# Kernel optimization log

Measured on AMD Instinct MI355X. Metric: run time of the kernel, lower is better.

## Reference

```python
import jax, jax.numpy as jnp
import numpy as np

T, H, NH, NKV, HD = 2048, 1024, 16, 4, 64
I, E, TOPK = 2048, 8, 2
EPS = 1e-5
ROPE_BASE = 10000.0


def rms_norm(x, w):
    var = jnp.mean(x * x, axis=-1, keepdims=True)
    return x * jax.lax.rsqrt(var + EPS) * w


def apply_rope(x, positions, n_heads):
    # neox-style rotary over full head_dim
    t = x.reshape(-1, n_heads, HD)
    half = HD // 2
    inv_freq = 1.0 / (ROPE_BASE ** (jnp.arange(0, half, dtype=jnp.float32) / half))
    freqs = positions.astype(jnp.float32)[:, None] * inv_freq[None, :]  # [T, half]
    cos = jnp.cos(freqs)[:, None, :]
    sin = jnp.sin(freqs)[:, None, :]
    x1, x2 = t[..., :half], t[..., half:]
    rot = jnp.concatenate([x1 * cos - x2 * sin, x2 * cos + x1 * sin], axis=-1)
    return rot.reshape(x.shape)


def setup_inputs():
    key = jax.random.key(0)
    ks = jax.random.split(key, 9)
    s = 0.02
    return dict(
        positions=jnp.arange(T, dtype=jnp.int32),
        hidden_states=jax.random.normal(ks[0], (T, H), jnp.float32),
        input_ln_w=jnp.ones((H,), jnp.float32),
        post_ln_w=jnp.ones((H,), jnp.float32),
        residual_ln_w=jnp.ones((H,), jnp.float32),
        qkv_w=jax.random.normal(ks[1], ((NH + 2 * NKV) * HD, H), jnp.float32) * s,
        o_w=jax.random.normal(ks[2], (H, NH * HD), jnp.float32) * s,
        gate_w=jax.random.normal(ks[3], (E, H), jnp.float32) * s,
        ws=jax.random.normal(ks[4], (E, 2 * I, H), jnp.float32) * s,
        w2s=jax.random.normal(ks[5], (E, H, I), jnp.float32) * s,
        res_w13=jax.random.normal(ks[6], (2 * H, H), jnp.float32) * s,
        res_w2=jax.random.normal(ks[7], (H, H), jnp.float32) * s,
    )


def attention(x, positions, qkv_w, o_w):
    qkv = x @ qkv_w.T  # [T, (NH+2*NKV)*HD]
    q, k, v = jnp.split(qkv, [NH * HD, NH * HD + NKV * HD], axis=-1)
    q = apply_rope(q, positions, NH)
    k = apply_rope(k, positions, NKV)
    q = q.reshape(T, NH, HD)
    k = k.reshape(T, NKV, HD)
    v = v.reshape(T, NKV, HD)
    rep = NH // NKV  # GQA: repeat kv heads
    k = jnp.repeat(k, rep, axis=1)
    v = jnp.repeat(v, rep, axis=1)
    scale = HD ** -0.5
    scores = jnp.einsum('tnd,snd->nts', q, k) * scale  # [NH, T, T]
    causal = jnp.tril(jnp.ones((T, T), dtype=bool))
    scores = jnp.where(causal[None], scores, -jnp.inf)
    probs = jax.nn.softmax(scores, axis=-1)
    out = jnp.einsum('nts,snd->tnd', probs, v).reshape(T, NH * HD)
    return out @ o_w.T


def silu_and_mul(gu):
    g, u = jnp.split(gu, 2, axis=-1)
    return jax.nn.silu(g) * u


def moe(x, gate_w, ws, w2s):
    logits = x @ gate_w.T  # [T, E]
    probs = jax.nn.softmax(logits, axis=-1)
    topk_w, topk_ids = jax.lax.top_k(probs, TOPK)
    topk_w = topk_w / jnp.sum(topk_w, axis=-1, keepdims=True)  # renormalize (top_k > 1)
    routes = jnp.zeros((x.shape[0], E), x.dtype).at[
        jnp.arange(x.shape[0])[:, None], topk_ids].set(topk_w)  # [T, E] sparse routing
    gu = jnp.einsum('th,eih->tei', x, ws)        # [T, E, 2I]
    act = silu_and_mul(gu)                        # [T, E, I]
    eo = jnp.einsum('tei,ehi->teh', act, w2s)     # [T, E, H]
    return jnp.einsum('te,teh->th', routes, eo)


def reference(positions, hidden_states, input_ln_w, post_ln_w, residual_ln_w,
              qkv_w, o_w, gate_w, ws, w2s, res_w13, res_w2):
    residual_input = hidden_states
    h = rms_norm(hidden_states, input_ln_w)
    h = attention(h, positions, qkv_w, o_w)
    residual_attn = residual_input + h
    # parallel residual MLP branch (ffn_dim == hidden)
    r = rms_norm(residual_attn, residual_ln_w)
    r = silu_and_mul(r @ res_w13.T) @ res_w2.T
    residual_mlp = residual_attn + r
    # MoE branch
    m = rms_norm(residual_attn, post_ln_w)
    m = moe(m, gate_w, ws, w2s)
    return residual_mlp + m
```

## Files before the change

### kernel.cpp

```cpp
#include <hip/hip_runtime.h>
#include <stdint.h>


typedef _Float16 f16;
typedef _Float16 f16x8 __attribute__((ext_vector_type(8)));
typedef _Float16 f16x4 __attribute__((ext_vector_type(4)));
typedef float f32x4 __attribute__((ext_vector_type(4)));

#define DEV __device__ __forceinline__

DEV void glds16(const void* g, void* l) {
  __builtin_amdgcn_global_load_lds((const __attribute__((address_space(1))) void*)g,
                                   (__attribute__((address_space(3))) void*)l, 16, 0, 0);
}

__global__ void cvt_f16_kernel(const float* __restrict__ in, f16* __restrict__ outp) {
  const size_t i = ((size_t)blockIdx.x * 256 + threadIdx.x) * 4;
  float4 f = *(const float4*)(in + i);
  f16x4 o;
  o[0] = (f16)f.x; o[1] = (f16)f.y; o[2] = (f16)f.z; o[3] = (f16)f.w;
  *(f16x4*)(outp + i) = o;
}

__global__ void cvt_f16x2_kernel(const float* __restrict__ in,
                                 f16* __restrict__ oh, f16* __restrict__ ol) {
  const size_t i = ((size_t)blockIdx.x * 256 + threadIdx.x) * 4;
  float4 f = *(const float4*)(in + i);
  f16x4 h, l;
  h[0] = (f16)f.x; l[0] = (f16)(f.x - (float)h[0]);
  h[1] = (f16)f.y; l[1] = (f16)(f.y - (float)h[1]);
  h[2] = (f16)f.z; l[2] = (f16)(f.z - (float)h[2]);
  h[3] = (f16)f.w; l[3] = (f16)(f.w - (float)h[3]);
  *(f16x4*)(oh + i) = h;
  *(f16x4*)(ol + i) = l;
}

__global__ void rmsnorm_kernel(const float* __restrict__ in, const float* __restrict__ w,
                               f16* __restrict__ outp) {
  const int t = blockIdx.x * 4 + (threadIdx.x >> 6);
  const int lane = threadIdx.x & 63;
  const float* x = in + (size_t)t * 1024;
  float v[16]; float ss = 0.f;
#pragma unroll
  for (int j = 0; j < 16; j++) { float a = x[lane + 64 * j]; v[j] = a; ss += a * a; }
#pragma unroll
  for (int m = 1; m < 64; m <<= 1) ss += __shfl_xor(ss, m);
  const float rs = rsqrtf(ss * (1.f / 1024.f) + 1e-5f);
#pragma unroll
  for (int j = 0; j < 16; j++)
    outp[(size_t)t * 1024 + lane + 64 * j] = (f16)(v[j] * rs * w[lane + 64 * j]);
}

__global__ void rmsnorm_dual_kernel(const float* __restrict__ in,
                                    const float* __restrict__ w1, const float* __restrict__ w2,
                                    f16* __restrict__ o1, f16* __restrict__ o2) {
  const int t = blockIdx.x * 4 + (threadIdx.x >> 6);
  const int lane = threadIdx.x & 63;
  const float* x = in + (size_t)t * 1024;
  float v[16]; float ss = 0.f;
#pragma unroll
  for (int j = 0; j < 16; j++) { float a = x[lane + 64 * j]; v[j] = a; ss += a * a; }
#pragma unroll
  for (int m = 1; m < 64; m <<= 1) ss += __shfl_xor(ss, m);
  const float rs = rsqrtf(ss * (1.f / 1024.f) + 1e-5f);
#pragma unroll
  for (int j = 0; j < 16; j++) {
    float nv = v[j] * rs;
    size_t idx = (size_t)t * 1024 + lane + 64 * j;
    o1[idx] = (f16)(nv * w1[lane + 64 * j]);
    o2[idx] = (f16)(nv * w2[lane + 64 * j]);
  }
}

template <int EPI, int BN, int SPLITK = 1>
__global__ __launch_bounds__(256) void gemm_f16_kernel(
    const f16* __restrict__ A, const f16* __restrict__ B,
    void* __restrict__ outp, const float* __restrict__ addsrc,
    int M, int N, int K) {
  constexpr int JT = BN / 32;
  constexpr int L = (BN == 128) ? 4 : 3;
  __shared__ __attribute__((aligned(16))) f16 As[3][128 * 32];
  __shared__ __attribute__((aligned(16))) f16 Bs[3][BN * 32];
  const int tid = threadIdx.x;
  const size_t row0 = (size_t)blockIdx.y * 128, col0 = (size_t)blockIdx.x * BN;
  const int ks = (SPLITK > 1) ? (int)blockIdx.z : 0;
  const int kspan = K / SPLITK, kb = ks * kspan;
  const int nt = kspan >> 5;
  const int c0 = tid, c1 = tid + 256;
  const int sw0 = ((c0 & 3) ^ ((c0 >> 3) & 3)) * 8;
  const int sw1 = ((c1 & 3) ^ ((c1 >> 3) & 3)) * 8;
  const f16* a0 = A + (row0 + (c0 >> 2)) * K + sw0;
  const f16* a1 = A + (row0 + (c1 >> 2)) * K + sw1;
  const f16* b0 = B + (col0 + (c0 >> 2)) * K + sw0;
  const f16* b1 = B + (col0 + ((BN == 128) ? (c1 >> 2) : 0)) * K + ((BN == 128) ? sw1 : 0);

  const int wave = tid >> 6, lane = tid & 63, lr = lane >> 4, lc = lane & 15;
  const int wr = wave >> 1, wc = wave & 1;
  const int rsw = (lr ^ ((lc >> 1) & 3)) * 8;

  f32x4 acc[4][JT];
#pragma unroll
  for (int i = 0; i < 4; i++)
#pragma unroll
    for (int j = 0; j < JT; j++) acc[i][j] = (f32x4){0.f, 0.f, 0.f, 0.f};

  auto stage = [&](int k0, int buf) {
    glds16(a0 + k0, As[buf] + c0 * 8);
    glds16(a1 + k0, As[buf] + c1 * 8);
    glds16(b0 + k0, Bs[buf] + c0 * 8);
    if constexpr (BN == 128) glds16(b1 + k0, Bs[buf] + c1 * 8);
  };

  stage(kb, 0); stage(kb + 32, 1);
  for (int t = 0; t < nt; ++t) {
    if (t < nt - 1) asm volatile("s_waitcnt vmcnt(%0)" :: "n"(L) : "memory");
    else            asm volatile("s_waitcnt vmcnt(0)" ::: "memory");
    __builtin_amdgcn_s_barrier();
    asm volatile("" ::: "memory");
    if (t + 2 < nt) stage(kb + (t + 2) * 32, (t + 2) % 3);
    const f16* Ab = As[t % 3];
    const f16* Bb = Bs[t % 3];
    f16x8 af[4], bfr[JT];
#pragma unroll
    for (int i = 0; i < 4; i++)
      af[i] = *(const f16x8*)(Ab + (wr * 64 + i * 16 + lc) * 32 + rsw);
#pragma unroll
    for (int j = 0; j < JT; j++)
      bfr[j] = *(const f16x8*)(Bb + (wc * (BN / 2) + j * 16 + lc) * 32 + rsw);
#pragma unroll
    for (int i = 0; i < 4; i++)
#pragma unroll
      for (int j = 0; j < JT; j++)
        acc[i][j] = __builtin_amdgcn_mfma_f32_16x16x32_f16(af[i], bfr[j], acc[i][j], 0, 0, 0);
  }

#pragma unroll
  for (int i = 0; i < 4; i++)
#pragma unroll
    for (int j = 0; j < JT; j++) {
      const size_t rbase = row0 + wr * 64 + i * 16 + lr * 4;
      const size_t col = col0 + wc * (BN / 2) + j * 16 + lc;
#pragma unroll
      for (int r = 0; r < 4; r++) {
        size_t idx = (rbase + r) * N + col;
        if constexpr (SPLITK > 1) {
          ((float*)outp)[(size_t)ks * M * N + idx] = acc[i][j][r];
        } else if constexpr (EPI == 0) ((float*)outp)[idx] = acc[i][j][r];
        else if constexpr (EPI == 1) ((float*)outp)[idx] = acc[i][j][r] + addsrc[idx];
        else ((f16*)outp)[idx] = (f16)acc[i][j][r];
      }
    }
}

template <int SPLITK>
__global__ __launch_bounds__(256) void gemm_f16x2_add_kernel(
    const f16* __restrict__ Ah, const f16* __restrict__ Al,
    const f16* __restrict__ Bh, const f16* __restrict__ Bl,
    float* __restrict__ outp, const float* __restrict__ addsrc,
    int M, int N, int K) {
  __shared__ __attribute__((aligned(16))) f16 Ash[3][128 * 32];
  __shared__ __attribute__((aligned(16))) f16 Asl[3][128 * 32];
  __shared__ __attribute__((aligned(16))) f16 Bsh[3][64 * 32];
  __shared__ __attribute__((aligned(16))) f16 Bsl[3][64 * 32];
  const int tid = threadIdx.x;
  const size_t row0 = (size_t)blockIdx.y * 128, col0 = (size_t)blockIdx.x * 64;
  const int ks = (SPLITK > 1) ? (int)blockIdx.z : 0;
  const int kspan = K / SPLITK, kb = ks * kspan;
  const int nt = kspan >> 5;
  const int c0 = tid, c1 = tid + 256;
  const int sw0 = ((c0 & 3) ^ ((c0 >> 3) & 3)) * 8;
  const int sw1 = ((c1 & 3) ^ ((c1 >> 3) & 3)) * 8;
  const size_t aoff0 = (row0 + (c0 >> 2)) * K + sw0;
  const size_t aoff1 = (row0 + (c1 >> 2)) * K + sw1;
  const size_t boff0 = (col0 + (c0 >> 2)) * K + sw0;

  const int wave = tid >> 6, lane = tid & 63, lr = lane >> 4, lc = lane & 15;
  const int wr = wave >> 1, wc = wave & 1;
  const int rsw = (lr ^ ((lc >> 1) & 3)) * 8;

  f32x4 acc[4][2];
#pragma unroll
  for (int i = 0; i < 4; i++)
#pragma unroll
    for (int j = 0; j < 2; j++) acc[i][j] = (f32x4){0.f, 0.f, 0.f, 0.f};

  auto stage = [&](int k0, int buf) {
    glds16(Ah + aoff0 + k0, Ash[buf] + c0 * 8);
    glds16(Ah + aoff1 + k0, Ash[buf] + c1 * 8);
    glds16(Al + aoff0 + k0, Asl[buf] + c0 * 8);
    glds16(Al + aoff1 + k0, Asl[buf] + c1 * 8);
    glds16(Bh + boff0 + k0, Bsh[buf] + c0 * 8);
    glds16(Bl + boff0 + k0, Bsl[buf] + c0 * 8);
  };

  stage(kb, 0); stage(kb + 32, 1);
  for (int t = 0; t < nt; ++t) {
    if (t < nt - 1) asm volatile("s_waitcnt vmcnt(%0)" :: "n"(6) : "memory");
    else            asm volatile("s_waitcnt vmcnt(0)" ::: "memory");
    __builtin_amdgcn_s_barrier();
    asm volatile("" ::: "memory");
    if (t + 2 < nt) stage(kb + (t + 2) * 32, (t + 2) % 3);
    const int bc = t % 3;
    f16x8 afh[4], afl[4], bfh[2], bfl[2];
#pragma unroll
    for (int i = 0; i < 4; i++) {
      const int ro = (wr * 64 + i * 16 + lc) * 32 + rsw;
      afh[i] = *(const f16x8*)(Ash[bc] + ro);
      afl[i] = *(const f16x8*)(Asl[bc] + ro);
    }
#pragma unroll
    for (int j = 0; j < 2; j++) {
      const int ro = (wc * 32 + j * 16 + lc) * 32 + rsw;
      bfh[j] = *(const f16x8*)(Bsh[bc] + ro);
      bfl[j] = *(const f16x8*)(Bsl[bc] + ro);
    }
#pragma unroll
    for (int i = 0; i < 4; i++)
#pragma unroll
      for (int j = 0; j < 2; j++) {
        acc[i][j] = __builtin_amdgcn_mfma_f32_16x16x32_f16(afh[i], bfh[j], acc[i][j], 0, 0, 0);
        acc[i][j] = __builtin_amdgcn_mfma_f32_16x16x32_f16(afh[i], bfl[j], acc[i][j], 0, 0, 0);
        acc[i][j] = __builtin_amdgcn_mfma_f32_16x16x32_f16(afl[i], bfh[j], acc[i][j], 0, 0, 0);
      }
  }

#pragma unroll
  for (int i = 0; i < 4; i++)
#pragma unroll
    for (int j = 0; j < 2; j++) {
      const size_t rbase = row0 + wr * 64 + i * 16 + lr * 4;
      const size_t col = col0 + wc * 32 + j * 16 + lc;
#pragma unroll
      for (int r = 0; r < 4; r++) {
        size_t idx = (rbase + r) * N + col;
        if constexpr (SPLITK > 1) outp[(size_t)ks * M * N + idx] = acc[i][j][r];
        else outp[idx] = acc[i][j][r] + addsrc[idx];
      }
    }
}

__global__ __launch_bounds__(256) void gemm_moe_gated_kernel(
    const f16* __restrict__ A, const f16* __restrict__ Ball, f16* __restrict__ actm,
    const int* __restrict__ perm, const int* __restrict__ counts,
    int K, size_t strideB) {
  const int e = (int)blockIdx.z;
  const int cnt = counts[e];
  const int bm = blockIdx.y;
  if (bm * 128 >= cnt) return;
  const int nt = K >> 5;
  const f16* B = Ball + (size_t)e * strideB;
  __shared__ __attribute__((aligned(16))) f16 As[3][128 * 32];
  __shared__ __attribute__((aligned(16))) f16 Bgs[3][64 * 32];
  __shared__ __attribute__((aligned(16))) f16 Bus[3][64 * 32];
  const int tid = threadIdx.x;
  const size_t col0 = (size_t)blockIdx.x * 64;
  const int c0 = tid, c1 = tid + 256;
  const int pbase = e * 2048 + bm * 128;
  const int rt0 = c0 >> 2, rt1 = c1 >> 2;
  const int sid0 = (bm * 128 + rt0 < cnt) ? perm[pbase + rt0] : 0;
  const int sid1 = (bm * 128 + rt1 < cnt) ? perm[pbase + rt1] : 0;
  const size_t ar0 = (size_t)(sid0 >> 1);
  const size_t ar1 = (size_t)(sid1 >> 1);
  const int sw0 = ((c0 & 3) ^ ((c0 >> 3) & 3)) * 8;
  const int sw1 = ((c1 & 3) ^ ((c1 >> 3) & 3)) * 8;
  const f16* ap0 = A + ar0 * K + sw0;
  const f16* ap1 = A + ar1 * K + sw1;
  const f16* bg0 = B + (col0 + (c0 >> 2)) * K + sw0;
  const f16* bu0 = B + (2048 + col0 + (c0 >> 2)) * K + sw0;

  const int wave = tid >> 6, lane = tid & 63, lr = lane >> 4, lc = lane & 15;
  const int wr = wave >> 1, wc = wave & 1;
  const int rsw = (lr ^ ((lc >> 1) & 3)) * 8;

  f32x4 accg[4][2], accu[4][2];
#pragma unroll
  for (int i = 0; i < 4; i++)
#pragma unroll
    for (int j = 0; j < 2; j++) {
      accg[i][j] = (f32x4){0.f, 0.f, 0.f, 0.f};
      accu[i][j] = (f32x4){0.f, 0.f, 0.f, 0.f};
    }

  auto stage = [&](int k0, int buf) {
    glds16(ap0 + k0, As[buf] + c0 * 8);
    glds16(ap1 + k0, As[buf] + c1 * 8);
    glds16(bg0 + k0, Bgs[buf] + c0 * 8);
    glds16(bu0 + k0, Bus[buf] + c0 * 8);
  };

  stage(0, 0); stage(32, 1);
  for (int t = 0; t < nt; ++t) {
    if (t < nt - 1) asm volatile("s_waitcnt vmcnt(%0)" :: "n"(4) : "memory");
    else            asm volatile("s_waitcnt vmcnt(0)" ::: "memory");
    __builtin_amdgcn_s_barrier();
    asm volatile("" ::: "memory");
    if (t + 2 < nt) stage((t + 2) * 32, (t + 2) % 3);
    const f16* Ab = As[t % 3];
    const f16* Bgb = Bgs[t % 3];
    const f16* Bub = Bus[t % 3];
    f16x8 af[4], bg[2], bu[2];
#pragma unroll
    for (int i = 0; i < 4; i++)
      af[i] = *(const f16x8*)(Ab + (wr * 64 + i * 16 + lc) * 32 + rsw);
#pragma unroll
    for (int j = 0; j < 2; j++) {
      const int ro = (wc * 32 + j * 16 + lc) * 32 + rsw;
      bg[j] = *(const f16x8*)(Bgb + ro);
      bu[j] = *(const f16x8*)(Bub + ro);
    }
    __builtin_amdgcn_s_setprio(1);
#pragma unroll
    for (int i = 0; i < 4; i++)
#pragma unroll
      for (int j = 0; j < 2; j++) {
        accg[i][j] = __builtin_amdgcn_mfma_f32_16x16x32_f16(af[i], bg[j], accg[i][j], 0, 0, 0);
        accu[i][j] = __builtin_amdgcn_mfma_f32_16x16x32_f16(af[i], bu[j], accu[i][j], 0, 0, 0);
      }
    __builtin_amdgcn_s_setprio(0);
  }

  int sids[4][4];
#pragma unroll
  for (int i = 0; i < 4; i++)
#pragma unroll
    for (int r = 0; r < 4; r++) {
      int rit = wr * 64 + i * 16 + lr * 4 + r;
      sids[i][r] = (bm * 128 + rit < cnt) ? perm[pbase + rit] : -1;
    }
#pragma unroll
  for (int i = 0; i < 4; i++)
#pragma unroll
    for (int j = 0; j < 2; j++) {
      const size_t col = col0 + wc * 32 + j * 16 + lc;
#pragma unroll
      for (int r = 0; r < 4; r++)
        if (sids[i][r] >= 0) {
          const float g = accg[i][j][r], u = accu[i][j][r];
          actm[(size_t)sids[i][r] * 2048 + col] = (f16)(g / (1.f + __expf(-g)) * u);
        }
    }
}

template <int DIVROW, int BN, int SPLITK = 1>
__global__ __launch_bounds__(256) void gemm_moe_kernel(
    const f16* __restrict__ A, const f16* __restrict__ Ball, void* __restrict__ outp,
    const int* __restrict__ perm, const int* __restrict__ counts,
    int N, int K, size_t strideB) {
  constexpr int JT = BN / 32;
  constexpr int L = (BN == 128) ? 4 : 3;
  const int e = (int)blockIdx.z / SPLITK;
  const int ks = (int)blockIdx.z % SPLITK;
  const int cnt = counts[e];
  const int bm = blockIdx.y;
  if (bm * 128 >= cnt) return;
  const int kspan = K / SPLITK, kb = ks * kspan;
  const int nt = kspan >> 5;
  const f16* B = Ball + (size_t)e * strideB;
  __shared__ __attribute__((aligned(16))) f16 As[3][128 * 32];
  __shared__ __attribute__((aligned(16))) f16 Bs[3][BN * 32];
  const int tid = threadIdx.x;
  const size_t col0 = (size_t)blockIdx.x * BN;
  const int c0 = tid, c1 = tid + 256;
  const int pbase = e * 2048 + bm * 128;
  const int rt0 = c0 >> 2, rt1 = c1 >> 2;
  const int sid0 = (bm * 128 + rt0 < cnt) ? perm[pbase + rt0] : 0;
  const int sid1 = (bm * 128 + rt1 < cnt) ? perm[pbase + rt1] : 0;
  const size_t ar0 = DIVROW ? (size_t)(sid0 >> 1) : (size_t)sid0;
  const size_t ar1 = DIVROW ? (size_t)(sid1 >> 1) : (size_t)sid1;
  const int sw0 = ((c0 & 3) ^ ((c0 >> 3) & 3)) * 8;
  const int sw1 = ((c1 & 3) ^ ((c1 >> 3) & 3)) * 8;
  const f16* ap0 = A + ar0 * K + sw0;
  const f16* ap1 = A + ar1 * K + sw1;
  const f16* b0 = B + (col0 + (c0 >> 2)) * K + sw0;
  const f16* b1 = B + (col0 + ((BN == 128) ? (c1 >> 2) : 0)) * K + ((BN == 128) ? sw1 : 0);

  const int wave = tid >> 6, lane = tid & 63, lr = lane >> 4, lc = lane & 15;
  const int wr = wave >> 1, wc = wave & 1;
  const int rsw = (lr ^ ((lc >> 1) & 3)) * 8;

  f32x4 acc[4][JT];
#pragma unroll
  for (int i = 0; i < 4; i++)
#pragma unroll
    for (int j = 0; j < JT; j++) acc[i][j] = (f32x4){0.f, 0.f, 0.f, 0.f};

  auto stage = [&](int k0, int buf) {
    glds16(ap0 + k0, As[buf] + c0 * 8);
    glds16(ap1 + k0, As[buf] + c1 * 8);
    glds16(b0 + k0, Bs[buf] + c0 * 8);
    if constexpr (BN == 128) glds16(b1 + k0, Bs[buf] + c1 * 8);
  };

  stage(kb, 0); stage(kb + 32, 1);
  for (int t = 0; t < nt; ++t) {
    if (t < nt - 1) asm volatile("s_waitcnt vmcnt(%0)" :: "n"(L) : "memory");
    else            asm volatile("s_waitcnt vmcnt(0)" ::: "memory");
    __builtin_amdgcn_s_barrier();
    asm volatile("" ::: "memory");
    if (t + 2 < nt) stage(kb + (t + 2) * 32, (t + 2) % 3);
    const f16* Ab = As[t % 3];
    const f16* Bb = Bs[t % 3];
    f16x8 af[4], bfr[JT];
#pragma unroll
    for (int i = 0; i < 4; i++)
      af[i] = *(const f16x8*)(Ab + (wr * 64 + i * 16 + lc) * 32 + rsw);
#pragma unroll
    for (int j = 0; j < JT; j++)
      bfr[j] = *(const f16x8*)(Bb + (wc * (BN / 2) + j * 16 + lc) * 32 + rsw);
    __builtin_amdgcn_s_setprio(1);
#pragma unroll
    for (int i = 0; i < 4; i++)
#pragma unroll
      for (int j = 0; j < JT; j++)
        acc[i][j] = __builtin_amdgcn_mfma_f32_16x16x32_f16(af[i], bfr[j], acc[i][j], 0, 0, 0);
    __builtin_amdgcn_s_setprio(0);
  }

  int sids[4][4];
#pragma unroll
  for (int i = 0; i < 4; i++)
#pragma unroll
    for (int r = 0; r < 4; r++) {
      int rit = wr * 64 + i * 16 + lr * 4 + r;
      sids[i][r] = (bm * 128 + rit < cnt) ? perm[pbase + rit] : -1;
    }
#pragma unroll
  for (int i = 0; i < 4; i++)
#pragma unroll
    for (int j = 0; j < JT; j++) {
      const size_t col = col0 + wc * (BN / 2) + j * 16 + lc;
#pragma unroll
      for (int r = 0; r < 4; r++)
        if (sids[i][r] >= 0) {
          if constexpr (SPLITK > 1)
            ((float*)outp)[((size_t)ks * 4096 + sids[i][r]) * N + col] = acc[i][j][r];
          else
            ((f16*)outp)[(size_t)sids[i][r] * N + col] = (f16)acc[i][j][r];
        }
    }
}

__global__ void rope_table_kernel(const int* __restrict__ pos, float2* __restrict__ tab) {
  const int idx = blockIdx.x * 256 + threadIdx.x;
  const int t = idx >> 5, i = idx & 31;
  const double ph = (double)pos[t] * exp((double)i * -0.28782313662425575);
  tab[idx] = make_float2((float)cos(ph), (float)sin(ph));
}

__global__ void rope_kernel(const float* __restrict__ qkv, const float2* __restrict__ tab,
                            f16* __restrict__ qr, f16* __restrict__ kr) {
  const int t = blockIdx.y;
  const int u = blockIdx.x * 256 + threadIdx.x;
  if (u >= 640) return;
  const float* b0 = qkv + (size_t)t * 1536;
  const float* b1 = b0 + (size_t)2048 * 1536;
  const int head = u >> 5, i = u & 31;
  const bool isq = head < 16;
  const int off = isq ? head * 64 + i : 1024 + (head - 16) * 64 + i;
  const float x1 = b0[off] + b1[off], x2 = b0[off + 32] + b1[off + 32];
  const float2 cs = tab[t * 32 + i];
  const float c = cs.x, s = cs.y;
  const float r1 = x1 * c - x2 * s, r2 = x2 * c + x1 * s;
  if (isq) {
    const float qs = 0.18033688011116042f;
    qr[(size_t)t * 1024 + head * 64 + i] = (f16)(qs * r1);
    qr[(size_t)t * 1024 + head * 64 + i + 32] = (f16)(qs * r2);
  } else {
    const int kh = head - 16;
    kr[(size_t)t * 256 + kh * 64 + i] = (f16)r1;
    kr[(size_t)t * 256 + kh * 64 + i + 32] = (f16)r2;
  }
}

__global__ void vtrans_kernel(const float* __restrict__ qkvf, f16* __restrict__ vt) {
  __shared__ float Ts[64 * 69];
  const int t0 = blockIdx.x * 64;
  const int kv = blockIdx.y;
  const int tid = threadIdx.x;
  const int tr = tid >> 2, jj = tid & 3;
  const float* src0 = qkvf + (size_t)(t0 + tr) * 1536 + 1280 + kv * 64 + jj * 16;
  const float* src1 = src0 + (size_t)2048 * 1536;
#pragma unroll
  for (int x = 0; x < 4; x++) {
    float4 f = *(const float4*)(src0 + x * 4);
    float4 g = *(const float4*)(src1 + x * 4);
    Ts[tr * 69 + jj * 16 + x * 4 + 0] = f.x + g.x;
    Ts[tr * 69 + jj * 16 + x * 4 + 1] = f.y + g.y;
    Ts[tr * 69 + jj * 16 + x * 4 + 2] = f.z + g.z;
    Ts[tr * 69 + jj * 16 + x * 4 + 3] = f.w + g.w;
  }
  __syncthreads();
  f16* dst = vt + (size_t)(kv * 64 + tr) * 2048 + t0 + jj * 16;
#pragma unroll
  for (int x = 0; x < 2; x++) {
    f16x8 o;
#pragma unroll
    for (int i = 0; i < 8; i++) o[i] = (f16)Ts[(jj * 16 + x * 8 + i) * 69 + tr];
    *(f16x8*)(dst + x * 8) = o;
  }
}

__global__ void add3_kernel(float* __restrict__ o, const float* __restrict__ a,
                            const float* __restrict__ p0, const float* __restrict__ p1) {
  const size_t i4 = ((size_t)blockIdx.x * 256 + threadIdx.x) * 4;
  float4 va = *(const float4*)(a + i4);
  float4 v0 = *(const float4*)(p0 + i4);
  float4 v1 = *(const float4*)(p1 + i4);
  va.x += v0.x + v1.x;
  va.y += v0.y + v1.y;
  va.z += v0.z + v1.z;
  va.w += v0.w + v1.w;
  *(float4*)(o + i4) = va;
}

__global__ __launch_bounds__(256, 3) void attn_kernel(
    const f16* __restrict__ qr, const f16* __restrict__ kr, const f16* __restrict__ vt,
    f16* __restrict__ ahi, f16* __restrict__ alo) {
  const int qt = 31 - (int)blockIdx.x;
  const int h = blockIdx.y;
  const int kvh = h >> 2;
  __shared__ __attribute__((aligned(16))) f16 Ks[128 * 72];
  __shared__ __attribute__((aligned(16))) f16 Vs[64 * 136];
  __shared__ __attribute__((aligned(16))) f16 Pl[4 * 16 * 136];
  const int tid = threadIdx.x;
  const int wave = tid >> 6, lane = tid & 63, lr = lane >> 4, lc = lane & 15;
  const int trow = qt * 64 + wave * 16 + lc;
  f16* Pw = Pl + wave * 16 * 136;

  const int krow = tid >> 3, kcol = (tid & 7) * 8;
  const int vrow = tid >> 4, vcol = (tid & 15) * 8;
  const f16* kgbase = kr + (size_t)kvh * 64 + kcol;
  const f16* vgbase = vt + (size_t)(kvh * 64 + vrow) * 2048 + vcol;

  const f16* qp = qr + (size_t)trow * 1024 + h * 64 + lr * 8;
  f16x8 qf0 = *(const f16x8*)(qp);
  f16x8 qf1 = *(const f16x8*)(qp + 32);

  float m_run = -3e38f, l_run = 0.f;
  f32x4 accO[4];
#pragma unroll
  for (int jo = 0; jo < 4; jo++) accO[jo] = (f32x4){0.f, 0.f, 0.f, 0.f};

  const int nch = (qt >> 1) + 1;

  f16x8 kreg[4], vreg[4];
#pragma unroll
  for (int it = 0; it < 4; it++) {
    kreg[it] = *(const f16x8*)(kgbase + (size_t)(it * 32 + krow) * 256);
    vreg[it] = *(const f16x8*)(vgbase + it * 16 * 2048);
  }

  for (int ch = 0; ch < nch; ++ch) {
    const int c0 = ch * 128;
    const bool last = (ch == nch - 1);

    __syncthreads();
#pragma unroll
    for (int it = 0; it < 4; it++) {
      *(f16x8*)(Ks + (it * 32 + krow) * 72 + kcol) = kreg[it];
      *(f16x8*)(Vs + (it * 16 + vrow) * 136 + vcol) = vreg[it];
    }
    __syncthreads();

    if (!last) {
      const int c1 = c0 + 128;
#pragma unroll
      for (int it = 0; it < 4; it++) {
        kreg[it] = *(const f16x8*)(kgbase + (size_t)(c1 + it * 32 + krow) * 256);
        vreg[it] = *(const f16x8*)(vgbase + it * 16 * 2048 + c1);
      }
    }

    f32x4 st[8];
    __builtin_amdgcn_s_setprio(1);
#pragma unroll
    for (int j = 0; j < 8; j++) {
      const f16* kp = Ks + (j * 16 + lc) * 72 + lr * 8;
      f16x8 ka0 = *(const f16x8*)(kp);
      f16x8 ka1 = *(const f16x8*)(kp + 32);
      f32x4 s = (f32x4){0.f, 0.f, 0.f, 0.f};
      s = __builtin_amdgcn_mfma_f32_16x16x32_f16(ka0, qf0, s, 0, 0, 0);
      s = __builtin_amdgcn_mfma_f32_16x16x32_f16(ka1, qf1, s, 0, 0, 0);
      st[j] = s;
    }
    __builtin_amdgcn_s_setprio(0);

    if (last) {
#pragma unroll
      for (int j = 0; j < 8; j++)
#pragma unroll
        for (int r = 0; r < 4; r++)
          if (c0 + j * 16 + lr * 4 + r > trow) st[j][r] = -3e38f;
    }

    float mc = -3e38f;
#pragma unroll
    for (int j = 0; j < 8; j++)
      mc = fmaxf(mc, fmaxf(fmaxf(st[j][0], st[j][1]), fmaxf(st[j][2], st[j][3])));
    mc = fmaxf(mc, __shfl_xor(mc, 16));
    mc = fmaxf(mc, __shfl_xor(mc, 32));
    const float mn = fmaxf(m_run, mc);
    const float alpha = __builtin_amdgcn_exp2f(m_run - mn);
    m_run = mn;

    float ls = 0.f;
#pragma unroll
    for (int j = 0; j < 8; j++) {
      f16x4 pv;
#pragma unroll
      for (int r = 0; r < 4; r++) {
        float e = __builtin_amdgcn_exp2f(st[j][r] - mn);
        ls += e;
        pv[r] = (f16)e;
      }
      *(f16x4*)(Pw + lc * 136 + j * 16 + lr * 4) = pv;
    }
    ls += __shfl_xor(ls, 16);
    ls += __shfl_xor(ls, 32);
    l_run = l_run * alpha + ls;
#pragma unroll
    for (int jo = 0; jo < 4; jo++) accO[jo] *= alpha;

    __builtin_amdgcn_s_setprio(1);
#pragma unroll
    for (int kkt = 0; kkt < 4; kkt++) {
      f16x8 pb = *(const f16x8*)(Pw + lc * 136 + kkt * 32 + lr * 8);
#pragma unroll
      for (int jo = 0; jo < 4; jo++) {
        f16x8 va = *(const f16x8*)(Vs + (jo * 16 + lc) * 136 + kkt * 32 + lr * 8);
        accO[jo] = __builtin_amdgcn_mfma_f32_16x16x32_f16(va, pb, accO[jo], 0, 0, 0);
      }
    }
    __builtin_amdgcn_s_setprio(0);
  }

  const float inv = 1.f / l_run;
#pragma unroll
  for (int jo = 0; jo < 4; jo++) {
    f16x4 hi4, lo4;
#pragma unroll
    for (int r = 0; r < 4; r++) {
      float o = accO[jo][r] * inv;
      f16 hv = (f16)o;
      hi4[r] = hv;
      lo4[r] = (f16)(o - (float)hv);
    }
    const size_t idx = (size_t)trow * 1024 + h * 64 + jo * 16 + lr * 4;
    *(f16x4*)(ahi + idx) = hi4;
    *(f16x4*)(alo + idx) = lo4;
  }
}

__global__ void routing_kernel(const float* __restrict__ resA,
                               const float* __restrict__ postw,
                               const float* __restrict__ gw,
                               int* __restrict__ counts, int* __restrict__ perm,
                               float* __restrict__ rw) {
  const int t = blockIdx.x * 4 + (threadIdx.x >> 6);
  const int lane = threadIdx.x & 63;
  const float* x = resA + (size_t)t * 1024;
  float v[16]; float ss = 0.f;
#pragma unroll
  for (int j = 0; j < 16; j++) { float a = x[lane + 64 * j]; v[j] = a; ss += a * a; }
#pragma unroll
  for (int m = 1; m < 64; m <<= 1) ss += __shfl_xor(ss, m);
  const float rs = rsqrtf(ss * (1.f / 1024.f) + 1e-5f);
#pragma unroll
  for (int j = 0; j < 16; j++) v[j] *= rs * postw[lane + 64 * j];
  float lg[8];
#pragma unroll
  for (int e = 0; e < 8; e++) {
    float p = 0.f;
    const float* g = gw + (size_t)e * 1024;
#pragma unroll
    for (int j = 0; j < 16; j++) p += v[j] * g[lane + 64 * j];
#pragma unroll
    for (int m = 1; m < 64; m <<= 1) p += __shfl_xor(p, m);
    lg[e] = p;
  }
  if (lane == 0) {
    int e0 = 0; float b0 = lg[0];
#pragma unroll
    for (int e = 1; e < 8; e++) if (lg[e] > b0) { b0 = lg[e]; e0 = e; }
    int e1 = -1; float b1 = -3e38f;
#pragma unroll
    for (int e = 0; e < 8; e++) if (e != e0 && lg[e] > b1) { b1 = lg[e]; e1 = e; }
    const float w0 = 1.f / (1.f + expf(b1 - b0));
    const float w1 = 1.f - w0;
    int p0 = atomicAdd(&counts[e0], 1);
    perm[e0 * 2048 + p0] = t * 2;
    int p1 = atomicAdd(&counts[e1], 1);
    perm[e1 * 2048 + p1] = t * 2 + 1;
    rw[t * 2] = w0;
    rw[t * 2 + 1] = w1;
  }
}

__global__ void silu_mul_kernel(const f16* __restrict__ gu, f16* __restrict__ outp, int lgN) {
  const int N = 1 << lgN;
  const size_t i4 = ((size_t)blockIdx.x * 256 + threadIdx.x) * 4;
  const size_t r = i4 >> lgN;
  const int c = (int)(i4 & (N - 1));
  const f16* gp = gu + r * (size_t)(2 * N) + c;
  f16x4 g = *(const f16x4*)gp;
  f16x4 u = *(const f16x4*)(gp + N);
  f16x4 o;
#pragma unroll
  for (int x = 0; x < 4; x++) {
    float gg = (float)g[x], uu = (float)u[x];
    o[x] = (f16)(gg / (1.f + __expf(-gg)) * uu);
  }
  *(f16x4*)(outp + r * (size_t)N + c) = o;
}

__global__ void final_add2_kernel(float* __restrict__ outp, const float* __restrict__ eo2,
                                  const float* __restrict__ rw) {
  const size_t i4 = ((size_t)blockIdx.x * 256 + threadIdx.x) * 4;
  const int t = (int)(i4 >> 10);
  const int c = (int)(i4 & 1023);
  const float w0 = rw[2 * t], w1 = rw[2 * t + 1];
  float4 s0 = {0.f, 0.f, 0.f, 0.f}, s1 = {0.f, 0.f, 0.f, 0.f};
#pragma unroll
  for (int ks = 0; ks < 2; ks++) {
    const float* p = eo2 + (size_t)ks * 4096 * 1024;
    float4 a = *(const float4*)(p + (size_t)(2 * t) * 1024 + c);
    float4 b = *(const float4*)(p + (size_t)(2 * t + 1) * 1024 + c);
    s0.x += a.x; s0.y += a.y; s0.z += a.z; s0.w += a.w;
    s1.x += b.x; s1.y += b.y; s1.z += b.z; s1.w += b.w;
  }
  float4 o = *(float4*)(outp + i4);
  o.x += w0 * s0.x + w1 * s1.x;
  o.y += w0 * s0.y + w1 * s1.y;
  o.z += w0 * s0.z + w1 * s1.z;
  o.w += w0 * s0.w + w1 * s1.w;
  *(float4*)(outp + i4) = o;
}

extern "C" void kernel_launch(void* const* d_in, const int* in_sizes, int n_in,
                              void* d_out, int out_size, void* d_ws, size_t ws_size,
                              hipStream_t stream) {
  const int* positions = (const int*)d_in[0];
  const float* hidden = (const float*)d_in[1];
  const float* in_ln = (const float*)d_in[2];
  const float* post_ln = (const float*)d_in[3];
  const float* res_ln = (const float*)d_in[4];
  const float* qkv_w = (const float*)d_in[5];
  const float* o_w = (const float*)d_in[6];
  const float* gate_w = (const float*)d_in[7];
  const float* ws_w = (const float*)d_in[8];
  const float* w2s_w = (const float*)d_in[9];
  const float* w13_w = (const float*)d_in[10];
  const float* w2_w = (const float*)d_in[11];
  float* out = (float*)d_out;

  char* p = (char*)d_ws;
  auto alloc = [&](size_t b) { void* r = (void*)p; p += (b + 255) & ~(size_t)255; return r; };

  f16* wqkv = (f16*)alloc((size_t)1536 * 1024 * 2);
  f16* woh  = (f16*)alloc((size_t)1024 * 1024 * 2);
  f16* wol  = (f16*)alloc((size_t)1024 * 1024 * 2);
  f16* wws  = (f16*)alloc((size_t)8 * 4096 * 1024 * 2);
  f16* ww2  = (f16*)alloc((size_t)8 * 1024 * 2048 * 2);
  f16* w13  = (f16*)alloc((size_t)2048 * 1024 * 2);
  f16* w2c  = (f16*)alloc((size_t)1024 * 1024 * 2);
  f16* hn   = (f16*)alloc((size_t)2048 * 1024 * 2);
  float* qkvp = (float*)alloc((size_t)2 * 2048 * 1536 * 4);
  float2* ptab = (float2*)alloc((size_t)2048 * 32 * 8);
  f16* qr = (f16*)alloc((size_t)2048 * 1024 * 2);
  f16* kr = (f16*)alloc((size_t)2048 * 256 * 2);
  f16* vt = (f16*)alloc((size_t)256 * 2048 * 2);
  f16* ath = (f16*)alloc((size_t)2048 * 1024 * 2);
  f16* atl = (f16*)alloc((size_t)2048 * 1024 * 2);
  float* opp = (float*)alloc((size_t)2 * 2048 * 1024 * 4);
  float* resA = (float*)alloc((size_t)2048 * 1024 * 4);
  f16* rn = (f16*)alloc((size_t)2048 * 1024 * 2);
  f16* mn = (f16*)alloc((size_t)2048 * 1024 * 2);
  f16* gu13 = (f16*)alloc((size_t)2048 * 2048 * 2);
  f16* act13 = (f16*)alloc((size_t)2048 * 1024 * 2);
  float* w2p = (float*)alloc((size_t)2 * 2048 * 1024 * 4);
  f16* actm = (f16*)alloc((size_t)4096 * 2048 * 2);
  float* eo2 = (float*)alloc((size_t)2 * 4096 * 1024 * 4);
  float* rw = (float*)alloc((size_t)4096 * 4);
  int* counts = (int*)alloc(256);
  int* perm = (int*)alloc((size_t)8 * 2048 * 4);

  cvt_f16_kernel<<<dim3(1536 * 1024 / 1024), dim3(256), 0, stream>>>(qkv_w, wqkv);
  cvt_f16_kernel<<<dim3(8 * 4096 * 1024 / 1024), dim3(256), 0, stream>>>(ws_w, wws);
  cvt_f16_kernel<<<dim3(8 * 1024 * 2048 / 1024), dim3(256), 0, stream>>>(w2s_w, ww2);
  cvt_f16_kernel<<<dim3(2048 * 1024 / 1024), dim3(256), 0, stream>>>(w13_w, w13);
  cvt_f16_kernel<<<dim3(1024 * 1024 / 1024), dim3(256), 0, stream>>>(w2_w, w2c);
  cvt_f16x2_kernel<<<dim3(1024 * 1024 / 1024), dim3(256), 0, stream>>>(o_w, woh, wol);
  rope_table_kernel<<<dim3(256), dim3(256), 0, stream>>>(positions, ptab);
  hipMemsetAsync(counts, 0, 256, stream);

  rmsnorm_kernel<<<dim3(512), dim3(256), 0, stream>>>(hidden, in_ln, hn);
  gemm_f16_kernel<0, 64, 2><<<dim3(24, 16, 2), dim3(256), 0, stream>>>(
      hn, wqkv, (void*)qkvp, (const float*)nullptr, 2048, 1536, 1024);
  rope_kernel<<<dim3(3, 2048), dim3(256), 0, stream>>>(qkvp, ptab, qr, kr);
  vtrans_kernel<<<dim3(32, 4), dim3(256), 0, stream>>>(qkvp, vt);
  attn_kernel<<<dim3(32, 16), dim3(256), 0, stream>>>(qr, kr, vt, ath, atl);
  gemm_f16x2_add_kernel<2><<<dim3(16, 16, 2), dim3(256), 0, stream>>>(
      ath, atl, woh, wol, opp, (const float*)nullptr, 2048, 1024, 1024);
  add3_kernel<<<dim3(2048), dim3(256), 0, stream>>>(
      resA, hidden, opp, opp + (size_t)2048 * 1024);

  rmsnorm_dual_kernel<<<dim3(512), dim3(256), 0, stream>>>(resA, res_ln, post_ln, rn, mn);
  routing_kernel<<<dim3(512), dim3(256), 0, stream>>>(resA, post_ln, gate_w, counts, perm, rw);

  gemm_f16_kernel<2, 64><<<dim3(32, 16), dim3(256), 0, stream>>>(
      rn, w13, (void*)gu13, (const float*)nullptr, 2048, 2048, 1024);
  silu_mul_kernel<<<dim3(2048 * 1024 / 1024), dim3(256), 0, stream>>>(gu13, act13, 10);
  gemm_f16_kernel<0, 64, 2><<<dim3(16, 16, 2), dim3(256), 0, stream>>>(
      act13, w2c, (void*)w2p, (const float*)nullptr, 2048, 1024, 1024);
  add3_kernel<<<dim3(2048), dim3(256), 0, stream>>>(
      out, resA, w2p, w2p + (size_t)2048 * 1024);

  gemm_moe_gated_kernel<<<dim3(32, 16, 8), dim3(256), 0, stream>>>(
      mn, wws, actm, perm, counts, 1024, (size_t)4096 * 1024);
  gemm_moe_kernel<0, 128, 2><<<dim3(8, 16, 16), dim3(256), 0, stream>>>(
      actm, ww2, (void*)eo2, perm, counts, 1024, 2048, (size_t)1024 * 2048);
  final_add2_kernel<<<dim3(2048 * 1024 / 1024), dim3(256), 0, stream>>>(out, eo2, rw);
}
```

Before: 611.6 us.

## Read fp32 MoE expert weights directly in GEMMs and fuse routing into rmsnorm

Drops the separate fp32-to-fp16 conversion passes over both MoE expert weight tensors. The gated and down MoE GEMMs now stage fp32 weights into LDS with a new swizzle and convert them to f16 in registers before the MFMA. Routing logits and top-2 selection move into the dual rmsnorm kernel, so resA is read once instead of twice. In exchange, the GEMMs fetch twice the weight bytes per tile and use more LDS, which can lower occupancy. Only the experts' row tiles that hold tokens are read, so unused weight rows are never touched.

```diff
diff --git a/kernel.cpp b/kernel.cpp
--- a/kernel.cpp
+++ b/kernel.cpp
@@ -12,6 +12,15 @@
 DEV void glds16(const void* g, void* l) {
   __builtin_amdgcn_global_load_lds((const __attribute__((address_space(1))) void*)g,
                                    (__attribute__((address_space(3))) void*)l, 16, 0, 0);
+}
+
+DEV f16x8 cvt8(const float* p) {
+  f32x4 lo = *(const f32x4*)p;
+  f32x4 hi = *(const f32x4*)(p + 4);
+  f16x8 o;
+  o[0] = (f16)lo[0]; o[1] = (f16)lo[1]; o[2] = (f16)lo[2]; o[3] = (f16)lo[3];
+  o[4] = (f16)hi[0]; o[5] = (f16)hi[1]; o[6] = (f16)hi[2]; o[7] = (f16)hi[3];
+  return o;
 }
 
 __global__ void cvt_f16_kernel(const float* __restrict__ in, f16* __restrict__ outp) {
@@ -51,9 +60,10 @@
     outp[(size_t)t * 1024 + lane + 64 * j] = (f16)(v[j] * rs * w[lane + 64 * j]);
 }
 
-__global__ void rmsnorm_dual_kernel(const float* __restrict__ in,
-                                    const float* __restrict__ w1, const float* __restrict__ w2,
-                                    f16* __restrict__ o1, f16* __restrict__ o2) {
+__global__ void rmsnorm_dual_route_kernel(
+    const float* __restrict__ in, const float* __restrict__ w1, const float* __restrict__ w2,
+    const float* __restrict__ gw, f16* __restrict__ o1, f16* __restrict__ o2,
+    int* __restrict__ counts, int* __restrict__ perm, float* __restrict__ rw) {
   const int t = blockIdx.x * 4 + (threadIdx.x >> 6);
   const int lane = threadIdx.x & 63;
   const float* x = in + (size_t)t * 1024;
@@ -63,12 +73,42 @@
 #pragma unroll
   for (int m = 1; m < 64; m <<= 1) ss += __shfl_xor(ss, m);
   const float rs = rsqrtf(ss * (1.f / 1024.f) + 1e-5f);
+  float pv[16];
 #pragma unroll
   for (int j = 0; j < 16; j++) {
-    float nv = v[j] * rs;
+    const float w1j = w1[lane + 64 * j], w2j = w2[lane + 64 * j];
+    const float nv = v[j] * rs;
     size_t idx = (size_t)t * 1024 + lane + 64 * j;
-    o1[idx] = (f16)(nv * w1[lane + 64 * j]);
-    o2[idx] = (f16)(nv * w2[lane + 64 * j]);
+    o1[idx] = (f16)(nv * w1j);
+    o2[idx] = (f16)(nv * w2j);
+    pv[j] = v[j] * (rs * w2j);
+  }
+  float lg[8];
+#pragma unroll
+  for (int e = 0; e < 8; e++) {
+    float p = 0.f;
+    const float* g = gw + (size_t)e * 1024;
+#pragma unroll
+    for (int j = 0; j < 16; j++) p += pv[j] * g[lane + 64 * j];
+#pragma unroll
+    for (int m = 1; m < 64; m <<= 1) p += __shfl_xor(p, m);
+    lg[e] = p;
+  }
+  if (lane == 0) {
+    int e0 = 0; float b0 = lg[0];
+#pragma unroll
+    for (int e = 1; e < 8; e++) if (lg[e] > b0) { b0 = lg[e]; e0 = e; }
+    int e1 = -1; float b1 = -3e38f;
+#pragma unroll
+    for (int e = 0; e < 8; e++) if (e != e0 && lg[e] > b1) { b1 = lg[e]; e1 = e; }
+    const float w0 = 1.f / (1.f + expf(b1 - b0));
+    const float wq = 1.f - w0;
+    int p0 = atomicAdd(&counts[e0], 1);
+    perm[e0 * 2048 + p0] = t * 2;
+    int p1 = atomicAdd(&counts[e1], 1);
+    perm[e1 * 2048 + p1] = t * 2 + 1;
+    rw[t * 2] = w0;
+    rw[t * 2 + 1] = wq;
   }
 }
 
@@ -240,7 +280,7 @@
 }
 
 __global__ __launch_bounds__(256) void gemm_moe_gated_kernel(
-    const f16* __restrict__ A, const f16* __restrict__ Ball, f16* __restrict__ actm,
+    const f16* __restrict__ A, const float* __restrict__ Ball, f16* __restrict__ actm,
     const int* __restrict__ perm, const int* __restrict__ counts,
     int K, size_t strideB) {
   const int e = (int)blockIdx.z;
@@ -248,10 +288,10 @@
   const int bm = blockIdx.y;
   if (bm * 128 >= cnt) return;
   const int nt = K >> 5;
-  const f16* B = Ball + (size_t)e * strideB;
+  const float* B = Ball + (size_t)e * strideB;
   __shared__ __attribute__((aligned(16))) f16 As[3][128 * 32];
-  __shared__ __attribute__((aligned(16))) f16 Bgs[3][64 * 32];
-  __shared__ __attribute__((aligned(16))) f16 Bus[3][64 * 32];
+  __shared__ __attribute__((aligned(16))) float Bgs[3][64 * 32];
+  __shared__ __attribute__((aligned(16))) float Bus[3][64 * 32];
   const int tid = threadIdx.x;
   const size_t col0 = (size_t)blockIdx.x * 64;
   const int c0 = tid, c1 = tid + 256;
@@ -265,8 +305,10 @@
   const int sw1 = ((c1 & 3) ^ ((c1 >> 3) & 3)) * 8;
   const f16* ap0 = A + ar0 * K + sw0;
   const f16* ap1 = A + ar1 * K + sw1;
-  const f16* bg0 = B + (col0 + (c0 >> 2)) * K + sw0;
-  const f16* bu0 = B + (2048 + col0 + (c0 >> 2)) * K + sw0;
+  const int rB = c0 >> 3;
+  const int sB = (c0 & 7) ^ ((rB & 3) << 1);
+  const float* bg0 = B + (size_t)(col0 + rB) * K + sB * 4;
+  const float* bu0 = B + (size_t)(2048 + col0 + rB) * K + sB * 4;
 
   const int wave = tid >> 6, lane = tid & 63, lr = lane >> 4, lc = lane & 15;
   const int wr = wave >> 1, wc = wave & 1;
@@ -284,29 +326,32 @@
   auto stage = [&](int k0, int buf) {
     glds16(ap0 + k0, As[buf] + c0 * 8);
     glds16(ap1 + k0, As[buf] + c1 * 8);
-    glds16(bg0 + k0, Bgs[buf] + c0 * 8);
-    glds16(bu0 + k0, Bus[buf] + c0 * 8);
+    glds16(bg0 + k0, Bgs[buf] + c0 * 4);
+    glds16(bg0 + (size_t)32 * K + k0, Bgs[buf] + (c0 + 256) * 4);
+    glds16(bu0 + k0, Bus[buf] + c0 * 4);
+    glds16(bu0 + (size_t)32 * K + k0, Bus[buf] + (c0 + 256) * 4);
   };
 
   stage(0, 0); stage(32, 1);
   for (int t = 0; t < nt; ++t) {
-    if (t < nt - 1) asm volatile("s_waitcnt vmcnt(%0)" :: "n"(4) : "memory");
+    if (t < nt - 1) asm volatile("s_waitcnt vmcnt(%0)" :: "n"(6) : "memory");
     else            asm volatile("s_waitcnt vmcnt(0)" ::: "memory");
     __builtin_amdgcn_s_barrier();
     asm volatile("" ::: "memory");
     if (t + 2 < nt) stage((t + 2) * 32, (t + 2) % 3);
     const f16* Ab = As[t % 3];
-    const f16* Bgb = Bgs[t % 3];
-    const f16* Bub = Bus[t % 3];
+    const float* Bgb = Bgs[t % 3];
+    const float* Bub = Bus[t % 3];
     f16x8 af[4], bg[2], bu[2];
 #pragma unroll
     for (int i = 0; i < 4; i++)
       af[i] = *(const f16x8*)(Ab + (wr * 64 + i * 16 + lc) * 32 + rsw);
 #pragma unroll
     for (int j = 0; j < 2; j++) {
-      const int ro = (wc * 32 + j * 16 + lc) * 32 + rsw;
-      bg[j] = *(const f16x8*)(Bgb + ro);
-      bu[j] = *(const f16x8*)(Bub + ro);
+      const int rb = wc * 32 + j * 16 + lc;
+      const int po = ((2 * lr) ^ ((rb & 3) << 1)) * 4;
+      bg[j] = cvt8(Bgb + rb * 32 + po);
+      bu[j] = cvt8(Bub + rb * 32 + po);
     }
     __builtin_amdgcn_s_setprio(1);
 #pragma unroll
@@ -341,13 +386,11 @@
     }
 }
 
-template <int DIVROW, int BN, int SPLITK = 1>
-__global__ __launch_bounds__(256) void gemm_moe_kernel(
-    const f16* __restrict__ A, const f16* __restrict__ Ball, void* __restrict__ outp,
+__global__ __launch_bounds__(256) void gemm_moe_down_kernel(
+    const f16* __restrict__ A, const float* __restrict__ Ball, float* __restrict__ outp,
     const int* __restrict__ perm, const int* __restrict__ counts,
     int N, int K, size_t strideB) {
-  constexpr int JT = BN / 32;
-  constexpr int L = (BN == 128) ? 4 : 3;
+  constexpr int SPLITK = 2;
   const int e = (int)blockIdx.z / SPLITK;
   const int ks = (int)blockIdx.z % SPLITK;
   const int cnt = counts[e];
@@ -355,63 +398,69 @@
   if (bm * 128 >= cnt) return;
   const int kspan = K / SPLITK, kb = ks * kspan;
   const int nt = kspan >> 5;
-  const f16* B = Ball + (size_t)e * strideB;
+  const float* B = Ball + (size_t)e * strideB;
   __shared__ __attribute__((aligned(16))) f16 As[3][128 * 32];
-  __shared__ __attribute__((aligned(16))) f16 Bs[3][BN * 32];
+  __shared__ __attribute__((aligned(16))) float Bs[3][128 * 32];
   const int tid = threadIdx.x;
-  const size_t col0 = (size_t)blockIdx.x * BN;
+  const size_t col0 = (size_t)blockIdx.x * 128;
   const int c0 = tid, c1 = tid + 256;
   const int pbase = e * 2048 + bm * 128;
   const int rt0 = c0 >> 2, rt1 = c1 >> 2;
   const int sid0 = (bm * 128 + rt0 < cnt) ? perm[pbase + rt0] : 0;
   const int sid1 = (bm * 128 + rt1 < cnt) ? perm[pbase + rt1] : 0;
-  const size_t ar0 = DIVROW ? (size_t)(sid0 >> 1) : (size_t)sid0;
-  const size_t ar1 = DIVROW ? (size_t)(sid1 >> 1) : (size_t)sid1;
+  const size_t ar0 = (size_t)sid0;
+  const size_t ar1 = (size_t)sid1;
   const int sw0 = ((c0 & 3) ^ ((c0 >> 3) & 3)) * 8;
   const int sw1 = ((c1 & 3) ^ ((c1 >> 3) & 3)) * 8;
   const f16* ap0 = A + ar0 * K + sw0;
   const f16* ap1 = A + ar1 * K + sw1;
-  const f16* b0 = B + (col0 + (c0 >> 2)) * K + sw0;
-  const f16* b1 = B + (col0 + ((BN == 128) ? (c1 >> 2) : 0)) * K + ((BN == 128) ? sw1 : 0);
+  const int rB = c0 >> 3;
+  const int sB = (c0 & 7) ^ ((rB & 3) << 1);
+  const float* b0 = B + (size_t)(col0 + rB) * K + sB * 4;
 
   const int wave = tid >> 6, lane = tid & 63, lr = lane >> 4, lc = lane & 15;
   const int wr = wave >> 1, wc = wave & 1;
   const int rsw = (lr ^ ((lc >> 1) & 3)) * 8;
 
-  f32x4 acc[4][JT];
-#pragma unroll
-  for (int i = 0; i < 4; i++)
-#pragma unroll
-    for (int j = 0; j < JT; j++) acc[i][j] = (f32x4){0.f, 0.f, 0.f, 0.f};
+  f32x4 acc[4][4];
+#pragma unroll
+  for (int i = 0; i < 4; i++)
+#pragma unroll
+    for (int j = 0; j < 4; j++) acc[i][j] = (f32x4){0.f, 0.f, 0.f, 0.f};
 
   auto stage = [&](int k0, int buf) {
     glds16(ap0 + k0, As[buf] + c0 * 8);
     glds16(ap1 + k0, As[buf] + c1 * 8);
-    glds16(b0 + k0, Bs[buf] + c0 * 8);
-    if constexpr (BN == 128) glds16(b1 + k0, Bs[buf] + c1 * 8);
+    glds16(b0 + k0, Bs[buf] + c0 * 4);
+    glds16(b0 + (size_t)32 * K + k0, Bs[buf] + (c0 + 256) * 4);
+    glds16(b0 + (size_t)64 * K + k0, Bs[buf] + (c0 + 512) * 4);
+    glds16(b0 + (size_t)96 * K + k0, Bs[buf] + (c0 + 768) * 4);
   };
 
   stage(kb, 0); stage(kb + 32, 1);
   for (int t = 0; t < nt; ++t) {
-    if (t < nt - 1) asm volatile("s_waitcnt vmcnt(%0)" :: "n"(L) : "memory");
+    if (t < nt - 1) asm volatile("s_waitcnt vmcnt(%0)" :: "n"(6) : "memory");
     else            asm volatile("s_waitcnt vmcnt(0)" ::: "memory");
     __builtin_amdgcn_s_barrier();
     asm volatile("" ::: "memory");
     if (t + 2 < nt) stage(kb + (t + 2) * 32, (t + 2) % 3);
     const f16* Ab = As[t % 3];
-    const f16* Bb = Bs[t % 3];
-    f16x8 af[4], bfr[JT];
+    const float* Bb = Bs[t % 3];
+    f16x8 af[4], bfr[4];
 #pragma unroll
     for (int i = 0; i < 4; i++)
       af[i] = *(const f16x8*)(Ab + (wr * 64 + i * 16 + lc) * 32 + rsw);
 #pragma unroll
-    for (int j = 0; j < JT; j++)
-      bfr[j] = *(const f16x8*)(Bb + (wc * (BN / 2) + j * 16 + lc) * 32 + rsw);
+    for (int j = 0; j < 4; j++) {
+      const int rb = wc * 64 + j * 16 + lc;
+      const int po = ((2 * lr) ^ ((rb & 3) << 1)) * 4;
+      bfr[j] = cvt8(Bb + rb * 32 + po);
+    }
     __builtin_amdgcn_s_setprio(1);
 #pragma unroll
     for (int i = 0; i < 4; i++)
 #pragma unroll
-      for (int j = 0; j < JT; j++)
+      for (int j = 0; j < 4; j++)
         acc[i][j] = __builtin_amdgcn_mfma_f32_16x16x32_f16(af[i], bfr[j], acc[i][j], 0, 0, 0);
     __builtin_amdgcn_s_setprio(0);
   }
@@ -427,16 +476,12 @@
 #pragma unroll
   for (int i = 0; i < 4; i++)
 #pragma unroll
-    for (int j = 0; j < JT; j++) {
-      const size_t col = col0 + wc * (BN / 2) + j * 16 + lc;
+    for (int j = 0; j < 4; j++) {
+      const size_t col = col0 + wc * 64 + j * 16 + lc;
 #pragma unroll
       for (int r = 0; r < 4; r++)
-        if (sids[i][r] >= 0) {
-          if constexpr (SPLITK > 1)
-            ((float*)outp)[((size_t)ks * 4096 + sids[i][r]) * N + col] = acc[i][j][r];
-          else
-            ((f16*)outp)[(size_t)sids[i][r] * N + col] = (f16)acc[i][j][r];
-        }
+        if (sids[i][r] >= 0)
+          outp[((size_t)ks * 4096 + sids[i][r]) * N + col] = acc[i][j][r];
     }
 }
 
@@ -651,51 +696,6 @@
   }
 }
 
-__global__ void routing_kernel(const float* __restrict__ resA,
-                               const float* __restrict__ postw,
-                               const float* __restrict__ gw,
-                               int* __restrict__ counts, int* __restrict__ perm,
-                               float* __restrict__ rw) {
-  const int t = blockIdx.x * 4 + (threadIdx.x >> 6);
-  const int lane = threadIdx.x & 63;
-  const float* x = resA + (size_t)t * 1024;
-  float v[16]; float ss = 0.f;
-#pragma unroll
-  for (int j = 0; j < 16; j++) { float a = x[lane + 64 * j]; v[j] = a; ss += a * a; }
-#pragma unroll
-  for (int m = 1; m < 64; m <<= 1) ss += __shfl_xor(ss, m);
-  const float rs = rsqrtf(ss * (1.f / 1024.f) + 1e-5f);
-#pragma unroll
-  for (int j = 0; j < 16; j++) v[j] *= rs * postw[lane + 64 * j];
-  float lg[8];
-#pragma unroll
-  for (int e = 0; e < 8; e++) {
-    float p = 0.f;
-    const float* g = gw + (size_t)e * 1024;
-#pragma unroll
-    for (int j = 0; j < 16; j++) p += v[j] * g[lane + 64 * j];
-#pragma unroll
-    for (int m = 1; m < 64; m <<= 1) p += __shfl_xor(p, m);
-    lg[e] = p;
-  }
-  if (lane == 0) {
-    int e0 = 0; float b0 = lg[0];
-#pragma unroll
-    for (int e = 1; e < 8; e++) if (lg[e] > b0) { b0 = lg[e]; e0 = e; }
-    int e1 = -1; float b1 = -3e38f;
-#pragma unroll
-    for (int e = 0; e < 8; e++) if (e != e0 && lg[e] > b1) { b1 = lg[e]; e1 = e; }
-    const float w0 = 1.f / (1.f + expf(b1 - b0));
-    const float w1 = 1.f - w0;
-    int p0 = atomicAdd(&counts[e0], 1);
-    perm[e0 * 2048 + p0] = t * 2;
-    int p1 = atomicAdd(&counts[e1], 1);
-    perm[e1 * 2048 + p1] = t * 2 + 1;
-    rw[t * 2] = w0;
-    rw[t * 2 + 1] = w1;
-  }
-}
-
 __global__ void silu_mul_kernel(const f16* __restrict__ gu, f16* __restrict__ outp, int lgN) {
   const int N = 1 << lgN;
   const size_t i4 = ((size_t)blockIdx.x * 256 + threadIdx.x) * 4;
@@ -759,8 +759,6 @@
   f16* wqkv = (f16*)alloc((size_t)1536 * 1024 * 2);
   f16* woh  = (f16*)alloc((size_t)1024 * 1024 * 2);
   f16* wol  = (f16*)alloc((size_t)1024 * 1024 * 2);
-  f16* wws  = (f16*)alloc((size_t)8 * 4096 * 1024 * 2);
-  f16* ww2  = (f16*)alloc((size_t)8 * 1024 * 2048 * 2);
   f16* w13  = (f16*)alloc((size_t)2048 * 1024 * 2);
   f16* w2c  = (f16*)alloc((size_t)1024 * 1024 * 2);
   f16* hn   = (f16*)alloc((size_t)2048 * 1024 * 2);
@@ -785,8 +783,6 @@
   int* perm = (int*)alloc((size_t)8 * 2048 * 4);
 
   cvt_f16_kernel<<<dim3(1536 * 1024 / 1024), dim3(256), 0, stream>>>(qkv_w, wqkv);
-  cvt_f16_kernel<<<dim3(8 * 4096 * 1024 / 1024), dim3(256), 0, stream>>>(ws_w, wws);
-  cvt_f16_kernel<<<dim3(8 * 1024 * 2048 / 1024), dim3(256), 0, stream>>>(w2s_w, ww2);
   cvt_f16_kernel<<<dim3(2048 * 1024 / 1024), dim3(256), 0, stream>>>(w13_w, w13);
   cvt_f16_kernel<<<dim3(1024 * 1024 / 1024), dim3(256), 0, stream>>>(w2_w, w2c);
   cvt_f16x2_kernel<<<dim3(1024 * 1024 / 1024), dim3(256), 0, stream>>>(o_w, woh, wol);
@@ -804,8 +800,8 @@
   add3_kernel<<<dim3(2048), dim3(256), 0, stream>>>(
       resA, hidden, opp, opp + (size_t)2048 * 1024);
 
-  rmsnorm_dual_kernel<<<dim3(512), dim3(256), 0, stream>>>(resA, res_ln, post_ln, rn, mn);
-  routing_kernel<<<dim3(512), dim3(256), 0, stream>>>(resA, post_ln, gate_w, counts, perm, rw);
+  rmsnorm_dual_route_kernel<<<dim3(512), dim3(256), 0, stream>>>(
+      resA, res_ln, post_ln, gate_w, rn, mn, counts, perm, rw);
 
   gemm_f16_kernel<2, 64><<<dim3(32, 16), dim3(256), 0, stream>>>(
       rn, w13, (void*)gu13, (const float*)nullptr, 2048, 2048, 1024);
@@ -816,8 +812,8 @@
       out, resA, w2p, w2p + (size_t)2048 * 1024);
 
   gemm_moe_gated_kernel<<<dim3(32, 16, 8), dim3(256), 0, stream>>>(
-      mn, wws, actm, perm, counts, 1024, (size_t)4096 * 1024);
-  gemm_moe_kernel<0, 128, 2><<<dim3(8, 16, 16), dim3(256), 0, stream>>>(
-      actm, ww2, (void*)eo2, perm, counts, 1024, 2048, (size_t)1024 * 2048);
+      mn, ws_w, actm, perm, counts, 1024, (size_t)4096 * 1024);
+  gemm_moe_down_kernel<<<dim3(8, 16, 16), dim3(256), 0, stream>>>(
+      actm, w2s_w, eo2, perm, counts, 1024, 2048, (size_t)1024 * 2048);
   final_add2_kernel<<<dim3(2048 * 1024 / 1024), dim3(256), 0, stream>>>(out, eo2, rw);
 }
```

Measured after the change: 632.8 us. 3.5% more time.
